# Kernel optimization log

Measured on AMD Instinct MI355X. Metric: run time of the kernel, lower is better.

The kernel has to match this reference:

```python
import jax, jax.numpy as jnp
import numpy as np

NY, NX = 800, 700  # BEV grid from voxel_feature_shape[2], voxel_feature_shape[3]
NCH = 2            # voxel_feature_shape[1] + 1 = occupancy + intensity


def setup_inputs() -> dict:
    key = jax.random.key(0)
    N, T, B = 200000, 32, 16
    k1, k2, k3, k4, k5 = jax.random.split(key, 5)
    vox_feats = jax.random.normal(k1, (N, T, 5), dtype=jnp.float32)
    num_points = jax.random.randint(k2, (N,), 1, T + 1, dtype=jnp.int32)
    b = jax.random.randint(k3, (N, 1), 0, B, dtype=jnp.int32)
    y = jax.random.randint(k4, (N, 1), 0, NY, dtype=jnp.int32)
    x = jax.random.randint(k5, (N, 1), 0, NX, dtype=jnp.int32)
    z = jnp.zeros((N, 1), dtype=jnp.int32)
    coords = jnp.concatenate([b, z, y, x], axis=1)  # [N, 4] = (batch, z, y, x)
    return {"vox_feats": vox_feats, "num_points": num_points,
            "coords": coords, "batch_size": B}


def reference(vox_feats, num_points, coords, batch_size):
    # intensity: mean over points per voxel, last feature channel -> [N]
    intensity = vox_feats.mean(axis=1)[:, -1]
    # occupancy value is 1.0 for every non-empty voxel (ones_like(num_points))
    # fuse the per-batch loop into one global scatter with batch-offset indices
    flat = (coords[:, 0].astype(jnp.int32) * (NY * NX)
            + coords[:, 2].astype(jnp.int32) * NX
            + coords[:, 3].astype(jnp.int32))  # [N]
    occ = jnp.zeros((batch_size * NY * NX,), dtype=vox_feats.dtype).at[flat].set(1.0)
    inten = jnp.zeros((batch_size * NY * NX,), dtype=vox_feats.dtype).at[flat].set(intensity)
    # [B, 2, NY, NX]
    return jnp.stack([occ.reshape(batch_size, NY, NX),
                      inten.reshape(batch_size, NY, NX)], axis=1)
```

## Files before the change

### kernel.cpp

```cpp
#include <hip/hip_runtime.h>
#include <hip/hip_bf16.h>


#define PX_NY 800
#define PX_NX 700
#define PX_T  32
#define PX_C  5
#define ROW_F4 40
#define TILE   64
#define TILE_F4 (TILE * ROW_F4)
#define LPAD   33

__global__ void __launch_bounds__(256)
pixor_k1(const float4* __restrict__ vox4,
         const int4*   __restrict__ coords4,
         float*        __restrict__ intens,
         unsigned int* __restrict__ vote,
         float4*       __restrict__ out4,
         int N, int P, int zq) {
    __shared__ float lsl[TILE * LPAD];

    const int tid  = threadIdx.x;
    const int gtid = blockIdx.x * 256 + tid;
    const int nth  = gridDim.x * 256;

    const float4 z = make_float4(0.f, 0.f, 0.f, 0.f);
    for (int i = gtid; i < zq; i += nth) out4[i] = z;

    const int t      = blockIdx.x;
    const int base   = t * TILE_F4;
    const int totF4  = N * ROW_F4;

#pragma unroll
    for (int k = 0; k < 10; ++k) {
        int i  = k * 256 + tid;
        int gi = base + i;
        if (gi < totF4) {
            float4 f = vox4[gi];
            int row = i / ROW_F4;
            int j   = i - row * ROW_F4;
            int sub = j % 5;
            if (sub) {
                float v = (sub == 1) ? f.x
                        : (sub == 2) ? f.y
                        : (sub == 3) ? f.z : f.w;
                int tp = (4 * j + (sub - 1) - 4) / 5;
                lsl[row * LPAD + tp] = v;
            }
        }
    }
    __syncthreads();

    int row = tid >> 2, q = tid & 3;
    const float* rp = &lsl[row * LPAD + q * 8];
    float s = 0.f;
#pragma unroll
    for (int m = 0; m < 8; ++m) s += rp[m];
    s += __shfl_xor(s, 1);
    s += __shfl_xor(s, 2);

    int grow = t * TILE + row;
    if (q == 0 && grow < N) {
        float inten = s * (1.0f / (float)PX_T);
        intens[grow] = inten;

        int4 c4 = coords4[grow];
        unsigned cell = (unsigned)(c4.x * P + c4.z * PX_NX + c4.w);
        unsigned key  = (unsigned)(grow + 1);

        unsigned old = atomicCAS(vote + cell, 0u, key);
        while (old != 0u) {
            if ((old - 1u) < (unsigned)N && old >= key) break;
            unsigned prev = atomicCAS(vote + cell, old, key);
            if (prev == old) break;
            old = prev;
        }
    }
}

__global__ void __launch_bounds__(256)
pixor_k2(const int4*   __restrict__ coords4,
         const float*  __restrict__ intens,
         unsigned int* __restrict__ vote,
         float*        __restrict__ out,
         int N, int P) {
    int n = blockIdx.x * 256 + threadIdx.x;
    if (n >= N) return;

    int4 c4 = coords4[n];
    int yx = c4.z * PX_NX + c4.w;
    unsigned cell = (unsigned)(c4.x * P + yx);

    unsigned v = atomicAdd(vote + cell, 0u);
    if (v == (unsigned)(n + 1)) {
        int base = c4.x * (2 * P) + yx;
        out[base]     = 1.0f;
        out[base + P] = intens[n];
    }
}

extern "C" void kernel_launch(void* const* d_in, const int* in_sizes, int n_in,
                              void* d_out, int out_size, void* d_ws, size_t ws_size,
                              hipStream_t stream) {
    const float* vox    = (const float*)d_in[0];
    const int*   coords = (const int*)d_in[2];
    float* out = (float*)d_out;

    const int N  = in_sizes[1];
    const int P  = PX_NY * PX_NX;
    const int B  = out_size / (2 * P);
    const int zq = out_size / 4;

    unsigned int* ws_vote = (unsigned int*)d_ws;
    float*        ws_int  = (float*)d_ws + (size_t)B * P;

    const int BLK = 256;
    const int ntiles = (N + TILE - 1) / TILE;

    pixor_k1<<<ntiles, BLK, 0, stream>>>((const float4*)vox, (const int4*)coords,
                                         ws_int, ws_vote, (float4*)out,
                                         N, P, zq);

    pixor_k2<<<(N + BLK - 1) / BLK, BLK, 0, stream>>>((const int4*)coords,
                                                      ws_int, ws_vote, out,
                                                      N, P);
}
```

Measured before the change: 45.27 us.

## Zero output with hipMemsetAsync and pack cell+intensity into one 64-bit record

Output zeroing moves out of the first kernel's grid-stride loop into a hipMemsetAsync. The separate intensity buffer and the coords re-read in the second kernel are replaced by one 64-bit record per voxel holding the cell index and the intensity bits. The second kernel then derives the output offset from the cell with a division, which cuts its loads to one 8-byte read per voxel. It adds an extra memset launch and relies on the workspace being large enough for the records.

```diff
diff --git a/kernel.cpp b/kernel.cpp
--- a/kernel.cpp
+++ b/kernel.cpp
@@ -4,6 +4,7 @@
 
 #define PX_NY 800
 #define PX_NX 700
+#define PX_P  (PX_NY * PX_NX)
 #define PX_T  32
 #define PX_C  5
 #define ROW_F4 40
@@ -12,22 +13,15 @@
 #define LPAD   33
 
 __global__ void __launch_bounds__(256)
-pixor_k1(const float4* __restrict__ vox4,
-         const int4*   __restrict__ coords4,
-         float*        __restrict__ intens,
-         unsigned int* __restrict__ vote,
-         float4*       __restrict__ out4,
-         int N, int P, int zq) {
+pixor_k1(const float4*       __restrict__ vox4,
+         const int4*         __restrict__ coords4,
+         unsigned long long* __restrict__ rec,
+         unsigned int*       __restrict__ vote,
+         int N) {
     __shared__ float lsl[TILE * LPAD];
 
-    const int tid  = threadIdx.x;
-    const int gtid = blockIdx.x * 256 + tid;
-    const int nth  = gridDim.x * 256;
-
-    const float4 z = make_float4(0.f, 0.f, 0.f, 0.f);
-    for (int i = gtid; i < zq; i += nth) out4[i] = z;
-
-    const int t      = blockIdx.x;
+    const int tid = threadIdx.x;
+    const int t   = blockIdx.x;
     const int base   = t * TILE_F4;
     const int totF4  = N * ROW_F4;
 
@@ -62,11 +56,13 @@
     int grow = t * TILE + row;
     if (q == 0 && grow < N) {
         float inten = s * (1.0f / (float)PX_T);
-        intens[grow] = inten;
 
         int4 c4 = coords4[grow];
-        unsigned cell = (unsigned)(c4.x * P + c4.z * PX_NX + c4.w);
+        unsigned cell = (unsigned)(c4.x * PX_P + c4.z * PX_NX + c4.w);
         unsigned key  = (unsigned)(grow + 1);
+
+        rec[grow] = ((unsigned long long)cell << 32) |
+                    (unsigned long long)__float_as_uint(inten);
 
         unsigned old = atomicCAS(vote + cell, 0u, key);
         while (old != 0u) {
@@ -79,23 +75,22 @@
 }
 
 __global__ void __launch_bounds__(256)
-pixor_k2(const int4*   __restrict__ coords4,
-         const float*  __restrict__ intens,
-         unsigned int* __restrict__ vote,
-         float*        __restrict__ out,
-         int N, int P) {
+pixor_k2(const unsigned long long* __restrict__ rec,
+         unsigned int*             __restrict__ vote,
+         float*                    __restrict__ out,
+         int N) {
     int n = blockIdx.x * 256 + threadIdx.x;
     if (n >= N) return;
 
-    int4 c4 = coords4[n];
-    int yx = c4.z * PX_NX + c4.w;
-    unsigned cell = (unsigned)(c4.x * P + yx);
+    unsigned long long r = rec[n];
+    unsigned cell = (unsigned)(r >> 32);
 
     unsigned v = atomicAdd(vote + cell, 0u);
     if (v == (unsigned)(n + 1)) {
-        int base = c4.x * (2 * P) + yx;
-        out[base]     = 1.0f;
-        out[base + P] = intens[n];
+        unsigned b    = cell / (unsigned)PX_P;
+        unsigned base = cell + b * (unsigned)PX_P;
+        out[base]        = 1.0f;
+        out[base + PX_P] = __uint_as_float((unsigned)r);
     }
 }
 
@@ -106,22 +101,20 @@
     const int*   coords = (const int*)d_in[2];
     float* out = (float*)d_out;
 
-    const int N  = in_sizes[1];
-    const int P  = PX_NY * PX_NX;
-    const int B  = out_size / (2 * P);
-    const int zq = out_size / 4;
+    const int N = in_sizes[1];
+    const int B = out_size / (2 * PX_P);
 
-    unsigned int* ws_vote = (unsigned int*)d_ws;
-    float*        ws_int  = (float*)d_ws + (size_t)B * P;
+    unsigned int*       ws_vote = (unsigned int*)d_ws;
+    unsigned long long* ws_rec  =
+        (unsigned long long*)((unsigned int*)d_ws + (size_t)B * PX_P + 32);
 
     const int BLK = 256;
     const int ntiles = (N + TILE - 1) / TILE;
 
+    hipMemsetAsync(d_out, 0, (size_t)out_size * sizeof(float), stream);
+
     pixor_k1<<<ntiles, BLK, 0, stream>>>((const float4*)vox, (const int4*)coords,
-                                         ws_int, ws_vote, (float4*)out,
-                                         N, P, zq);
+                                         ws_rec, ws_vote, N);
 
-    pixor_k2<<<(N + BLK - 1) / BLK, BLK, 0, stream>>>((const int4*)coords,
-                                                      ws_int, ws_vote, out,
-                                                      N, P);
+    pixor_k2<<<(N + BLK - 1) / BLK, BLK, 0, stream>>>(ws_rec, ws_vote, out, N);
 }
```

Result: slower. 50.60 us (+11.8%).
